# Performance work log

Hardware: AMD Instinct MI355X
Metric: run time of the kernel (lower is better)

## Reference

```python
import jax, jax.numpy as jnp
import numpy as np

BINS = 10


def setup_inputs() -> dict:
    key = jax.random.key(0)
    k1, k2 = jax.random.split(key)
    N, C = 4194304, 16
    inputs = jax.random.normal(k1, (N, C), dtype=jnp.float32)
    target = jax.random.randint(k2, (N,), 0, 2, dtype=jnp.int64)
    return {"inputs": inputs, "target": target}


def reference(inputs, target):
    N = inputs.shape[0]
    edges = jnp.arange(BINS + 1, dtype=inputs.dtype) / BINS  # [0, 0.1, ..., 1.0]

    # p_t = softmax(inputs)[i, target_i]
    logp = jax.nn.log_softmax(inputs, axis=1)
    p_t = jnp.take_along_axis(jnp.exp(logp), target[:, None], axis=1)[:, 0]

    # gradient norm g = |p_t - target| (detached in the original)
    g = jnp.abs(jax.lax.stop_gradient(p_t) - target.astype(inputs.dtype))

    # bin index: matches (g >= edges[i]) & (g < edges[i+1]); clip handles g == 1.0
    bin_idx = jnp.clip(jnp.searchsorted(edges, g, side="right") - 1, 0, BINS - 1)

    # per-bin counts via one scatter-add (replaces the per-bin CPU loop)
    counts = jax.ops.segment_sum(jnp.ones_like(g), bin_idx, num_segments=BINS)
    counts = jnp.maximum(counts, 1.0)  # occupied bins always have count >= 1

    # weights[i] = (N / bins) / num_in_bin(i)
    weights = (N / BINS) / counts[bin_idx]

    # weighted cross entropy, summed
    nll = -jnp.take_along_axis(logp, target[:, None], axis=1)[:, 0]
    return jnp.sum(nll * weights)
```

## Files before the change

kernel.cpp:

```cpp
#include <hip/hip_runtime.h>

#define BINS 10
#define GRID 2048
#define BLOCK 256
#define NWAVES (BLOCK / 64)

typedef float vfloat4 __attribute__((ext_vector_type(4)));

__global__ __launch_bounds__(BLOCK) void ghm_main(const float* __restrict__ x,
                                                  const int* __restrict__ tgt,
                                                  float* __restrict__ p_sum,
                                                  unsigned int* __restrict__ p_cnt,
                                                  int n_rows) {
    float h_sum[BINS];
    unsigned int h_cnt[BINS];
    #pragma unroll
    for (int b = 0; b < BINS; ++b) { h_sum[b] = 0.0f; h_cnt[b] = 0u; }

    const int gid = blockIdx.x * BLOCK + threadIdx.x;
    const int stride = GRID * BLOCK;
    const vfloat4* __restrict__ xv = (const vfloat4*)x;

    const float edges[BINS] = {0.1f, 0.2f, 0.3f, 0.4f, 0.5f,
                               0.6f, 0.7f, 0.8f, 0.9f, 1.0f};

    for (int r = gid; r < n_rows; r += stride) {
        const vfloat4 v0 = __builtin_nontemporal_load(&xv[(size_t)r * 4 + 0]);
        const vfloat4 v1 = __builtin_nontemporal_load(&xv[(size_t)r * 4 + 1]);
        const vfloat4 v2 = __builtin_nontemporal_load(&xv[(size_t)r * 4 + 2]);
        const vfloat4 v3 = __builtin_nontemporal_load(&xv[(size_t)r * 4 + 3]);
        const int tg = tgt[r];

        const vfloat4 vs = (tg < 8) ? ((tg < 4) ? v0 : v1) : ((tg < 12) ? v2 : v3);
        const int c = tg & 3;
        const float xt = (c < 2) ? ((c == 0) ? vs.x : vs.y) : ((c == 2) ? vs.z : vs.w);

        const float s =
            __expf(v0.x - xt) + __expf(v0.y - xt) + __expf(v0.z - xt) + __expf(v0.w - xt) +
            __expf(v1.x - xt) + __expf(v1.y - xt) + __expf(v1.z - xt) + __expf(v1.w - xt) +
            __expf(v2.x - xt) + __expf(v2.y - xt) + __expf(v2.z - xt) + __expf(v2.w - xt) +
            __expf(v3.x - xt) + __expf(v3.y - xt) + __expf(v3.z - xt) + __expf(v3.w - xt);

        const float nll = __logf(s);
        const float p = 1.0f / s;
        const float g = fabsf(p - (float)tg);

        int b = 0;
        #pragma unroll
        for (int k = 0; k < BINS; ++k) b += (g >= edges[k]) ? 1 : 0;
        b = (b > BINS - 1) ? (BINS - 1) : b;

        #pragma unroll
        for (int k = 0; k < BINS; ++k) {
            if (b == k) { h_sum[k] += nll; h_cnt[k] += 1u; }
        }
    }

    __shared__ float ls[NWAVES * BINS];
    __shared__ unsigned int lc[NWAVES * BINS];
    const int lane = threadIdx.x & 63;
    const int wv = threadIdx.x >> 6;
    #pragma unroll
    for (int b = 0; b < BINS; ++b) {
        float s = h_sum[b];
        unsigned int cn = h_cnt[b];
        #pragma unroll
        for (int off = 32; off > 0; off >>= 1) {
            s += __shfl_xor(s, off);
            cn += __shfl_xor(cn, off);
        }
        if (lane == 0) { ls[wv * BINS + b] = s; lc[wv * BINS + b] = cn; }
    }
    __syncthreads();

    if (threadIdx.x < BINS) {
        float s = 0.0f;
        unsigned int cn = 0u;
        #pragma unroll
        for (int w = 0; w < NWAVES; ++w) { s += ls[w * BINS + threadIdx.x]; cn += lc[w * BINS + threadIdx.x]; }
        p_sum[threadIdx.x * GRID + blockIdx.x] = s;
        p_cnt[threadIdx.x * GRID + blockIdx.x] = cn;
    }
}

__global__ void ghm_final(const float* __restrict__ p_sum,
                          const unsigned int* __restrict__ p_cnt,
                          float* __restrict__ out, int n_rows) {
    const int lane = threadIdx.x;
    double total = 0.0;
    for (int b = 0; b < BINS; ++b) {
        double s = 0.0;
        unsigned long long c = 0;
        for (int k = lane; k < GRID; k += 64) {
            s += (double)p_sum[b * GRID + k];
            c += (unsigned long long)p_cnt[b * GRID + k];
        }
        #pragma unroll
        for (int off = 32; off > 0; off >>= 1) {
            s += __shfl_xor(s, off);
            c += __shfl_xor(c, off);
        }
        double cd = (double)c;
        if (cd < 1.0) cd = 1.0;
        total += s / cd;
    }
    if (lane == 0) out[0] = (float)(total * ((double)n_rows / (double)BINS));
}

extern "C" void kernel_launch(void* const* d_in, const int* in_sizes, int n_in,
                              void* d_out, int out_size, void* d_ws, size_t ws_size,
                              hipStream_t stream) {
    const float* x = (const float*)d_in[0];
    const int* tgt = (const int*)d_in[1];
    const int n_rows = in_sizes[1];

    float* p_sum = (float*)d_ws;
    unsigned int* p_cnt = (unsigned int*)((char*)d_ws + BINS * GRID * sizeof(float));

    ghm_main<<<GRID, BLOCK, 0, stream>>>(x, tgt, p_sum, p_cnt, n_rows);
    ghm_final<<<1, 64, 0, stream>>>(p_sum, p_cnt, (float*)d_out, n_rows);
}
```

Before: 456.2 us.

## Split each row across a four-thread quad with coalesced float4 loads

Each row of 16 logits is now handled by four threads instead of one. Each thread loads one float4, so consecutive lanes read contiguous memory, and the nontemporal loads are dropped. The target logit is fetched with a lane shuffle and the exp-sum is reduced with two xor shuffles. Only the quad leader does the log, binning and histogram update. This is meant to improve load coalescing and memory parallelism, at the cost of extra shuffles, idle lanes during binning, four redundant target loads per row and four times more loop iterations per thread.

```diff
diff --git a/kernel.cpp b/kernel.cpp
--- a/kernel.cpp
+++ b/kernel.cpp
@@ -4,8 +4,6 @@
 #define GRID 2048
 #define BLOCK 256
 #define NWAVES (BLOCK / 64)
-
-typedef float vfloat4 __attribute__((ext_vector_type(4)));
 
 __global__ __launch_bounds__(BLOCK) void ghm_main(const float* __restrict__ x,
                                                   const int* __restrict__ tgt,
@@ -17,48 +15,45 @@
     #pragma unroll
     for (int b = 0; b < BINS; ++b) { h_sum[b] = 0.0f; h_cnt[b] = 0u; }
 
-    const int gid = blockIdx.x * BLOCK + threadIdx.x;
-    const int stride = GRID * BLOCK;
-    const vfloat4* __restrict__ xv = (const vfloat4*)x;
+    const int lane = threadIdx.x & 63;
+    const int j = threadIdx.x & 3;
+    const int quad0 = (blockIdx.x * BLOCK + threadIdx.x) >> 2;
+    const int quads_total = (GRID * BLOCK) >> 2;
+    const float4* __restrict__ xv = (const float4*)x;
 
     const float edges[BINS] = {0.1f, 0.2f, 0.3f, 0.4f, 0.5f,
                                0.6f, 0.7f, 0.8f, 0.9f, 1.0f};
 
-    for (int r = gid; r < n_rows; r += stride) {
-        const vfloat4 v0 = __builtin_nontemporal_load(&xv[(size_t)r * 4 + 0]);
-        const vfloat4 v1 = __builtin_nontemporal_load(&xv[(size_t)r * 4 + 1]);
-        const vfloat4 v2 = __builtin_nontemporal_load(&xv[(size_t)r * 4 + 2]);
-        const vfloat4 v3 = __builtin_nontemporal_load(&xv[(size_t)r * 4 + 3]);
+    for (int r = quad0; r < n_rows; r += quads_total) {
+        const float4 v = xv[(size_t)r * 4 + j];
         const int tg = tgt[r];
 
-        const vfloat4 vs = (tg < 8) ? ((tg < 4) ? v0 : v1) : ((tg < 12) ? v2 : v3);
         const int c = tg & 3;
-        const float xt = (c < 2) ? ((c == 0) ? vs.x : vs.y) : ((c == 2) ? vs.z : vs.w);
+        const float cand = (c < 2) ? ((c == 0) ? v.x : v.y) : ((c == 2) ? v.z : v.w);
+        const float xt = __shfl(cand, (lane & 60) + (tg >> 2));
 
-        const float s =
-            __expf(v0.x - xt) + __expf(v0.y - xt) + __expf(v0.z - xt) + __expf(v0.w - xt) +
-            __expf(v1.x - xt) + __expf(v1.y - xt) + __expf(v1.z - xt) + __expf(v1.w - xt) +
-            __expf(v2.x - xt) + __expf(v2.y - xt) + __expf(v2.z - xt) + __expf(v2.w - xt) +
-            __expf(v3.x - xt) + __expf(v3.y - xt) + __expf(v3.z - xt) + __expf(v3.w - xt);
+        float s = __expf(v.x - xt) + __expf(v.y - xt) + __expf(v.z - xt) + __expf(v.w - xt);
+        s += __shfl_xor(s, 1);
+        s += __shfl_xor(s, 2);
 
-        const float nll = __logf(s);
-        const float p = 1.0f / s;
-        const float g = fabsf(p - (float)tg);
+        if (j == 0) {
+            const float nll = __logf(s);
+            const float g = fabsf(1.0f / s - (float)tg);
 
-        int b = 0;
-        #pragma unroll
-        for (int k = 0; k < BINS; ++k) b += (g >= edges[k]) ? 1 : 0;
-        b = (b > BINS - 1) ? (BINS - 1) : b;
+            int b = 0;
+            #pragma unroll
+            for (int k = 0; k < BINS; ++k) b += (g >= edges[k]) ? 1 : 0;
+            b = (b > BINS - 1) ? (BINS - 1) : b;
 
-        #pragma unroll
-        for (int k = 0; k < BINS; ++k) {
-            if (b == k) { h_sum[k] += nll; h_cnt[k] += 1u; }
+            #pragma unroll
+            for (int k = 0; k < BINS; ++k) {
+                if (b == k) { h_sum[k] += nll; h_cnt[k] += 1u; }
+            }
         }
     }
 
     __shared__ float ls[NWAVES * BINS];
     __shared__ unsigned int lc[NWAVES * BINS];
-    const int lane = threadIdx.x & 63;
     const int wv = threadIdx.x >> 6;
     #pragma unroll
     for (int b = 0; b < BINS; ++b) {
```

New measurement: 452.8 us. About the same (-0.8%).
